# Kernel optimization log

Measured on AMD Instinct MI355X. Metric: run time of the kernel, lower is better.

Reference implementation:

```python
import jax, jax.numpy as jnp
import numpy as np

IMG_SIZE = 1024.0  # image width == height in pixels
N_PTS = 2_000_000


def setup_inputs() -> dict:
    key = jax.random.key(0)
    k1, k2, k3 = jax.random.split(key, 3)
    # 2D screen-space gaussian centers, pixel coords in [0, IMG_SIZE)
    pos2d = jax.random.uniform(k1, (N_PTS, 2), dtype=jnp.float32) * IMG_SIZE
    # PSD 2x2 covariances: A A^T + 0.5 I (screen-space extent of a few pixels)
    A = 0.8 * jax.random.normal(k2, (N_PTS, 2, 2), dtype=jnp.float32)
    cov2d = jnp.einsum('nij,nkj->nik', A, A) + 0.5 * jnp.eye(2, dtype=jnp.float32)
    opacity = jax.random.uniform(k3, (N_PTS,), dtype=jnp.float32)
    return {"pos2d": pos2d, "cov2d": cov2d, "opacity": opacity, "num_tile": 16}


def reference(pos2d, cov2d, opacity, num_tile):
    # --- per-gaussian rasterization setup (radius + conic) ---
    a = cov2d[:, 0, 0]; b = cov2d[:, 0, 1]
    c = cov2d[:, 1, 0]; d = cov2d[:, 1, 1]
    trace = a + d
    det = a * d - b * c
    term1 = 0.5 * trace
    term2 = 0.5 * jnp.sqrt(jnp.clip(trace * trace - 4.0 * det, 0.0))
    # max eigenvalue of the 2x2 covariance, as in GaussianRender.get_radius
    radius = jnp.maximum(term1 - term2, term1 + term2)
    inv_det = 1.0 / det
    conic = jnp.stack([d * inv_det, -b * inv_det, a * inv_det], axis=-1)  # [N,3]

    # --- tile binning (histogram) ---
    tile_size = IMG_SIZE / num_tile
    tile_xy = jnp.clip(jnp.floor(pos2d / tile_size).astype(jnp.int32), 0, num_tile - 1)
    tile_id = tile_xy[:, 1] * num_tile + tile_xy[:, 0]  # [N] in [0, num_tile^2)
    n_tiles = num_tile * num_tile
    tile_counts = jax.ops.segment_sum(
        jnp.ones_like(tile_id), tile_id, num_segments=n_tiles)  # [T^2]
    cum = jnp.cumsum(tile_counts)
    tile_offsets = jnp.concatenate([jnp.zeros((1,), cum.dtype), cum[:-1]])  # exclusive

    # --- counting sort: stable argsort by tile id reorders gaussians per tile ---
    order = jnp.argsort(tile_id)  # stable
    feat = jnp.concatenate(
        [pos2d, conic, opacity[:, None], radius[:, None]], axis=1)  # [N,7]
    sorted_feat = feat[order]
    return sorted_feat, tile_counts, tile_offsets, order.astype(jnp.int32)
```

## Files before the change

### kernel.cpp

```cpp
#include <hip/hip_runtime.h>

#define NT 16
#define NTILES 256
#define INV_TILE (1.0f/64.0f)
#define CHUNK 2048
#define THREADS 1024
#define NWAVES 16
#define FSTRIDE 2049

typedef float fv4 __attribute__((ext_vector_type(4)));

__device__ __forceinline__ int tile_of(float x, float y) {
    int tx = (int)floorf(x * INV_TILE);
    tx = tx < 0 ? 0 : (tx > NT - 1 ? NT - 1 : tx);
    int ty = (int)floorf(y * INV_TILE);
    ty = ty < 0 ? 0 : (ty > NT - 1 ? NT - 1 : ty);
    return ty * NT + tx;
}

__device__ __forceinline__ unsigned long long match_mask(int t, bool valid) {
    unsigned long long m = ~0ull;
#pragma unroll
    for (int b = 0; b < 8; ++b) {
        unsigned long long bal = __ballot((t >> b) & 1);
        m &= ((t >> b) & 1) ? bal : ~bal;
    }
    m &= __ballot(valid);
    return m;
}

__global__ __launch_bounds__(THREADS, 8) void k_hist(const float2* __restrict__ pos2d,
                                                     int* __restrict__ gTot,
                                                     int N) {
    __shared__ unsigned short cnt[NWAVES][NTILES];
    const int tid = threadIdx.x;
    const int wl = tid >> 6, lane = tid & 63;
    const int base_i = blockIdx.x * CHUNK;
    ((int*)cnt)[tid] = 0;
    ((int*)cnt)[tid + THREADS] = 0;
    __syncthreads();
#pragma unroll
    for (int r = 0; r < 2; ++r) {
        int o = wl * 128 + r * 64 + lane;
        int i = base_i + o;
        bool valid = i < N;
        int t = 0;
        if (valid) { float2 p = pos2d[i]; t = tile_of(p.x, p.y); }
        unsigned long long m = match_mask(t, valid);
        if (valid) {
            unsigned long long below = m & ((1ull << lane) - 1ull);
            if (below == 0ull)
                cnt[wl][t] = (unsigned short)(cnt[wl][t] + __popcll(m));
        }
    }
    __syncthreads();
    if (tid < NTILES) {
        int tot = 0;
#pragma unroll
        for (int w = 0; w < NWAVES; ++w) tot += cnt[w][tid];
        gTot[(size_t)blockIdx.x * NTILES + tid] = tot;
    }
}

__global__ __launch_bounds__(512) void k_scan(const int* __restrict__ gTot,
                                              int* __restrict__ gBaseT,
                                              int* __restrict__ gcnt,
                                              float* __restrict__ out_counts,
                                              int NWA) {
    const int t = blockIdx.x;
    const int tid = threadIdx.x;
    const int wl = tid >> 6, lane = tid & 63;
    __shared__ int wsum[8];

    int vals[4];
    const int base_row = tid * 4;
#pragma unroll
    for (int k = 0; k < 4; ++k) {
        int row = base_row + k;
        vals[k] = (row < NWA) ? gTot[(size_t)row * NTILES + t] : 0;
    }
    int tv = vals[0] + vals[1] + vals[2] + vals[3];
    int x = tv;
#pragma unroll
    for (int s = 1; s < 64; s <<= 1) {
        int y = __shfl_up(x, s);
        if (lane >= s) x += y;
    }
    if (lane == 63) wsum[wl] = x;
    __syncthreads();
    int wprefix = 0;
    for (int u = 0; u < wl; ++u) wprefix += wsum[u];
    int running = wprefix + (x - tv);
#pragma unroll
    for (int k = 0; k < 4; ++k) {
        int row = base_row + k;
        if (row < NWA) gBaseT[(size_t)t * NWA + row] = running;
        running += vals[k];
    }
    if (tid == 0) {
        int total = 0;
#pragma unroll
        for (int u = 0; u < 8; ++u) total += wsum[u];
        gcnt[t] = total;
        out_counts[t] = (float)total;
    }
}

__global__ __launch_bounds__(THREADS, 8) void k_scatter(const float2* __restrict__ pos2d,
                                                        const float4* __restrict__ cov2d,
                                                        const float*  __restrict__ opacity,
                                                        const int*    __restrict__ gBaseT,
                                                        const int*    __restrict__ gcnt,
                                                        float* __restrict__ out_feat,
                                                        float* __restrict__ out_offsets,
                                                        float* __restrict__ out_order,
                                                        int N, int NWA) {
    __shared__ float sFeat[7 * FSTRIDE];
    __shared__ unsigned int slotPk[CHUNK];
    __shared__ unsigned short cnt[NWAVES][NTILES];
    __shared__ int gbase[NTILES];
    __shared__ int base7[NTILES];
    __shared__ int obase[NTILES];
    __shared__ int wsum[NWAVES];

    const int tid = threadIdx.x;
    const int wl = tid >> 6, lane = tid & 63;
    const int b = blockIdx.x;

    const int nwg = gridDim.x;
    const int q = nwg >> 3, r = nwg & 7;
    const int xcd = b & 7, idx = b >> 3;
    const int chunk = (xcd < r ? xcd * (q + 1) : r * (q + 1) + (xcd - r) * q) + idx;
    const int base_i = chunk * CHUNK;

    ((int*)cnt)[tid] = 0;
    ((int*)cnt)[tid + THREADS] = 0;

    {
        int ct = 0, x = 0, gbt = 0;
        if (tid < NTILES) {
            gbt = gBaseT[(size_t)tid * NWA + chunk];
            ct = gcnt[tid];
            x = ct;
#pragma unroll
            for (int s = 1; s < 64; s <<= 1) {
                int y = __shfl_up(x, s);
                if (lane >= s) x += y;
            }
            if (lane == 63) wsum[wl] = x;
        }
        __syncthreads();
        if (tid < NTILES) {
            int wpre = 0;
            for (int u = 0; u < wl; ++u) wpre += wsum[u];
            int off = wpre + x - ct;
            gbase[tid] = off + gbt;
            if (b == 0) out_offsets[tid] = (float)off;
        }
    }
    __syncthreads();

    unsigned int meta[2];
#pragma unroll
    for (int r2 = 0; r2 < 2; ++r2) {
        int o = wl * 128 + r2 * 64 + lane;
        int i = base_i + o;
        bool valid = i < N;
        int t = 0;
        if (valid) {
            float2 p  = pos2d[i];
            fv4 cv = __builtin_nontemporal_load((const fv4*)cov2d + i);
            float op  = opacity[i];
            t = tile_of(p.x, p.y);
            float a = cv[0], bb = cv[1], d = cv[3];
            float trace = a + d;
            float det = a * d - bb * bb;
            float term1 = 0.5f * trace;
            float term2 = 0.5f * sqrtf(fmaxf(trace * trace - 4.0f * det, 0.0f));
            float rad = fmaxf(term1 - term2, term1 + term2);
            float inv = 1.0f / det;
            sFeat[0 * FSTRIDE + o] = p.x;
            sFeat[1 * FSTRIDE + o] = p.y;
            sFeat[2 * FSTRIDE + o] = d * inv;
            sFeat[3 * FSTRIDE + o] = -bb * inv;
            sFeat[4 * FSTRIDE + o] = a * inv;
            sFeat[5 * FSTRIDE + o] = op;
            sFeat[6 * FSTRIDE + o] = rad;
        }
        unsigned long long m = match_mask(t, valid);
        unsigned int pk = 0x80000000u;
        if (valid) {
            unsigned long long below = m & ((1ull << lane) - 1ull);
            int rank = __popcll(below);
            int b0 = cnt[wl][t];
            if (below == 0ull) cnt[wl][t] = (unsigned short)(b0 + __popcll(m));
            pk = ((unsigned)t << 16) | (unsigned)(b0 + rank);
        }
        meta[r2] = pk;
    }
    __syncthreads();

    int tot = 0, x = 0;
    if (tid < NTILES) {
#pragma unroll
        for (int w = 0; w < NWAVES; ++w) tot += cnt[w][tid];
        x = tot;
#pragma unroll
        for (int s = 1; s < 64; s <<= 1) {
            int y = __shfl_up(x, s);
            if (lane >= s) x += y;
        }
        if (lane == 63) wsum[wl] = x;
    }
    __syncthreads();
    if (tid < NTILES) {
        int wpre = 0;
        for (int u = 0; u < wl; ++u) wpre += wsum[u];
        int run = wpre + x - tot;
        int gb = gbase[tid];
        int ob = gb - run;
        obase[tid] = ob;
        base7[tid] = ob * 7;
#pragma unroll
        for (int w = 0; w < NWAVES; ++w) {
            int cw = cnt[w][tid];
            cnt[w][tid] = (unsigned short)run;
            run += cw;
        }
    }
    __syncthreads();

#pragma unroll
    for (int r2 = 0; r2 < 2; ++r2) {
        unsigned int pk = meta[r2];
        if (!(pk & 0x80000000u)) {
            int o = wl * 128 + r2 * 64 + lane;
            int t  = pk >> 16;
            int pw = pk & 0xFFFF;
            slotPk[cnt[wl][t] + pw] = ((unsigned)t << 16) | (unsigned)o;
        }
    }
    __syncthreads();

    int nvalid = N - base_i; if (nvalid > CHUNK) nvalid = CHUNK;
    int nv7 = nvalid * 7;
    {
        int j = (int)((unsigned)tid / 7u);
        int c = tid - 7 * j;
        for (int f = tid; f < nv7; f += THREADS) {
            unsigned int pk = slotPk[j];
            int t = pk >> 16;
            int o = pk & 0xFFFF;
            out_feat[(size_t)(base7[t] + f)] = sFeat[c * FSTRIDE + o];
            j += 146; c += 2;
            if (c >= 7) { c -= 7; j += 1; }
        }
    }
    for (int j2 = tid; j2 < nvalid; j2 += THREADS) {
        unsigned int pk = slotPk[j2];
        out_order[obase[pk >> 16] + j2] = (float)(base_i + (int)(pk & 0xFFFF));
    }
}

extern "C" void kernel_launch(void* const* d_in, const int* in_sizes, int n_in,
                              void* d_out, int out_size, void* d_ws, size_t ws_size,
                              hipStream_t stream) {
    const float2* pos2d   = (const float2*)d_in[0];
    const float4* cov2d   = (const float4*)d_in[1];
    const float*  opacity = (const float*)d_in[2];
    const int N = in_sizes[2];

    float* out         = (float*)d_out;
    float* out_feat    = out;
    float* out_counts  = out + (size_t)N * 7;
    float* out_offsets = out_counts + NTILES;
    float* out_order   = out_offsets + NTILES;

    int nchunks = (N + CHUNK - 1) / CHUNK;

    int* gTot   = (int*)d_ws;
    int* gBaseT = gTot + (size_t)nchunks * NTILES;
    int* gcnt   = gBaseT + (size_t)NTILES * nchunks;

    k_hist<<<nchunks, THREADS, 0, stream>>>(pos2d, gTot, N);
    k_scan<<<NTILES, 512, 0, stream>>>(gTot, gBaseT, gcnt, out_counts, nchunks);
    k_scatter<<<nchunks, THREADS, 0, stream>>>(pos2d, cov2d, opacity, gBaseT, gcnt,
                                               out_feat, out_offsets, out_order,
                                               N, nchunks);
}
```

Measured before the change: 131.9 us.

## Process two chunks per scatter block, prefetching the second chunk's inputs

```diff
diff --git a/kernel.cpp b/kernel.cpp
--- a/kernel.cpp
+++ b/kernel.cpp
@@ -105,6 +105,113 @@
         out_counts[t] = (float)total;
     }
 }
+
+#define PROCESS(PP, CC, OO, cc, PREFETCH)                                    \
+    {                                                                        \
+        const int base_i = (cc) * CHUNK;                                     \
+        ((int*)cnt)[tid] = 0;                                                \
+        ((int*)cnt)[tid + THREADS] = 0;                                      \
+        __syncthreads();   \
+        unsigned int meta[2];                                                \
+        _Pragma("unroll")                                                    \
+        for (int r2 = 0; r2 < 2; ++r2) {                                     \
+            int o = wl * 128 + r2 * 64 + lane;                               \
+            int i = base_i + o;                                              \
+            bool valid = ((cc) < NWA) && (i < N);                            \
+            int t = 0;                                                       \
+            if (valid) {                                                     \
+                float2 p = PP[r2]; fv4 cv = CC[r2]; float op = OO[r2];       \
+                t = tile_of(p.x, p.y);                                       \
+                float a = cv[0], bb2 = cv[1], d = cv[3];                     \
+                float trace = a + d;                                         \
+                float det = a * d - bb2 * bb2;       \
+                float term1 = 0.5f * trace;                                  \
+                float term2 = 0.5f * sqrtf(fmaxf(trace * trace - 4.0f * det, 0.0f)); \
+                float rad = fmaxf(term1 - term2, term1 + term2);             \
+                float inv = 1.0f / det;                                      \
+                sFeat[0 * FSTRIDE + o] = p.x;                                \
+                sFeat[1 * FSTRIDE + o] = p.y;                                \
+                sFeat[2 * FSTRIDE + o] = d * inv;                            \
+                sFeat[3 * FSTRIDE + o] = -bb2 * inv;                         \
+                sFeat[4 * FSTRIDE + o] = a * inv;                            \
+                sFeat[5 * FSTRIDE + o] = op;                                 \
+                sFeat[6 * FSTRIDE + o] = rad;                                \
+            }                                                                \
+            unsigned long long m = match_mask(t, valid);                     \
+            unsigned int pk = 0x80000000u;                                   \
+            if (valid) {                                                     \
+                unsigned long long below = m & ((1ull << lane) - 1ull);      \
+                int rank = __popcll(below);                                  \
+                int b0 = cnt[wl][t];         \
+                if (below == 0ull) cnt[wl][t] = (unsigned short)(b0 + __popcll(m)); \
+                pk = ((unsigned)t << 16) | (unsigned)(b0 + rank);            \
+            }                                                                \
+            meta[r2] = pk;                                                   \
+        }                                                                    \
+        __syncthreads();                                                     \
+        int tot = 0, x2 = 0;                                                 \
+        if (tid < NTILES) {                                                  \
+            _Pragma("unroll")                                                \
+            for (int w = 0; w < NWAVES; ++w) tot += cnt[w][tid];             \
+            x2 = tot;                                                        \
+            _Pragma("unroll")                                                \
+            for (int s = 1; s < 64; s <<= 1) {                               \
+                int y = __shfl_up(x2, s);                                    \
+                if (lane >= s) x2 += y;                                      \
+            }                                                                \
+            if (lane == 63) wsum[wl] = x2;                                   \
+        }                                                                    \
+        __syncthreads();                                                     \
+        if (tid < NTILES) {                                                  \
+            int wpre = 0;                                                    \
+            for (int u = 0; u < wl; ++u) wpre += wsum[u];                    \
+            int run = wpre + x2 - tot;                                       \
+            int gb = gbase[tid];                                             \
+            int ob = gb - run;                                               \
+            obase[tid] = ob;                                                 \
+            base7[tid] = ob * 7;                                             \
+            gbase[tid] = gb + tot;               \
+            _Pragma("unroll")                                                \
+            for (int w = 0; w < NWAVES; ++w) {                               \
+                int cw = cnt[w][tid];                                        \
+                cnt[w][tid] = (unsigned short)run;                           \
+                run += cw;                                                   \
+            }                                                                \
+        }                                                                    \
+        __syncthreads();                                                     \
+        _Pragma("unroll")                                                    \
+        for (int r2 = 0; r2 < 2; ++r2) {                                     \
+            unsigned int pk = meta[r2];                                      \
+            if (!(pk & 0x80000000u)) {                                       \
+                int o = wl * 128 + r2 * 64 + lane;                           \
+                int t = pk >> 16;                                            \
+                int pw = pk & 0xFFFF;                                        \
+                slotPk[cnt[wl][t] + pw] = ((unsigned)t << 16) | (unsigned)o; \
+            }                                                                \
+        }                                                                    \
+        __syncthreads();                                                     \
+        PREFETCH                                                             \
+        int nvalid = ((cc) < NWA) ? (N - base_i) : 0;                        \
+        if (nvalid > CHUNK) nvalid = CHUNK;                                  \
+        if (nvalid < 0) nvalid = 0;                                          \
+        int nv7 = nvalid * 7;                                                \
+        {                                                                    \
+            int j = (int)((unsigned)tid / 7u);   \
+            int c = tid - 7 * j;                                             \
+            for (int f = tid; f < nv7; f += THREADS) {                       \
+                unsigned int pk = slotPk[j];                                 \
+                int t = pk >> 16;                                            \
+                int o = pk & 0xFFFF;                                         \
+                out_feat[(size_t)(base7[t] + f)] = sFeat[c * FSTRIDE + o];   \
+                j += 146; c += 2;                                            \
+                if (c >= 7) { c -= 7; j += 1; }                              \
+            }                                                                \
+        }                                                                    \
+        for (int j2 = tid; j2 < nvalid; j2 += THREADS) {                     \
+            unsigned int pk = slotPk[j2];                                    \
+            out_order[obase[pk >> 16] + j2] = (float)(base_i + (int)(pk & 0xFFFF)); \
+        }                                                                    \
+    }
 
 __global__ __launch_bounds__(THREADS, 8) void k_scatter(const float2* __restrict__ pos2d,
                                                         const float4* __restrict__ cov2d,
@@ -130,16 +237,25 @@
     const int nwg = gridDim.x;
     const int q = nwg >> 3, r = nwg & 7;
     const int xcd = b & 7, idx = b >> 3;
-    const int chunk = (xcd < r ? xcd * (q + 1) : r * (q + 1) + (xcd - r) * q) + idx;
-    const int base_i = chunk * CHUNK;
-
-    ((int*)cnt)[tid] = 0;
-    ((int*)cnt)[tid + THREADS] = 0;
+    const int pair = (xcd < r ? xcd * (q + 1) : r * (q + 1) + (xcd - r) * q) + idx;
+    const int c0 = pair * 2;
+
+    float2 p0[2]; fv4 cv0[2]; float op0[2];
+    float2 p1[2]; fv4 cv1[2]; float op1[2];
+#pragma unroll
+    for (int r2 = 0; r2 < 2; ++r2) {
+        int i = c0 * CHUNK + wl * 128 + r2 * 64 + lane;
+        if (i < N) {
+            p0[r2]  = pos2d[i];
+            cv0[r2] = __builtin_nontemporal_load((const fv4*)cov2d + i);
+            op0[r2] = opacity[i];
+        }
+    }
 
     {
         int ct = 0, x = 0, gbt = 0;
         if (tid < NTILES) {
-            gbt = gBaseT[(size_t)tid * NWA + chunk];
+            gbt = gBaseT[(size_t)tid * NWA + c0];
             ct = gcnt[tid];
             x = ct;
 #pragma unroll
@@ -158,108 +274,20 @@
             if (b == 0) out_offsets[tid] = (float)off;
         }
     }
-    __syncthreads();
-
-    unsigned int meta[2];
-#pragma unroll
-    for (int r2 = 0; r2 < 2; ++r2) {
-        int o = wl * 128 + r2 * 64 + lane;
-        int i = base_i + o;
-        bool valid = i < N;
-        int t = 0;
-        if (valid) {
-            float2 p  = pos2d[i];
-            fv4 cv = __builtin_nontemporal_load((const fv4*)cov2d + i);
-            float op  = opacity[i];
-            t = tile_of(p.x, p.y);
-            float a = cv[0], bb = cv[1], d = cv[3];
-            float trace = a + d;
-            float det = a * d - bb * bb;
-            float term1 = 0.5f * trace;
-            float term2 = 0.5f * sqrtf(fmaxf(trace * trace - 4.0f * det, 0.0f));
-            float rad = fmaxf(term1 - term2, term1 + term2);
-            float inv = 1.0f / det;
-            sFeat[0 * FSTRIDE + o] = p.x;
-            sFeat[1 * FSTRIDE + o] = p.y;
-            sFeat[2 * FSTRIDE + o] = d * inv;
-            sFeat[3 * FSTRIDE + o] = -bb * inv;
-            sFeat[4 * FSTRIDE + o] = a * inv;
-            sFeat[5 * FSTRIDE + o] = op;
-            sFeat[6 * FSTRIDE + o] = rad;
-        }
-        unsigned long long m = match_mask(t, valid);
-        unsigned int pk = 0x80000000u;
-        if (valid) {
-            unsigned long long below = m & ((1ull << lane) - 1ull);
-            int rank = __popcll(below);
-            int b0 = cnt[wl][t];
-            if (below == 0ull) cnt[wl][t] = (unsigned short)(b0 + __popcll(m));
-            pk = ((unsigned)t << 16) | (unsigned)(b0 + rank);
-        }
-        meta[r2] = pk;
-    }
-    __syncthreads();
-
-    int tot = 0, x = 0;
-    if (tid < NTILES) {
-#pragma unroll
-        for (int w = 0; w < NWAVES; ++w) tot += cnt[w][tid];
-        x = tot;
-#pragma unroll
-        for (int s = 1; s < 64; s <<= 1) {
-            int y = __shfl_up(x, s);
-            if (lane >= s) x += y;
-        }
-        if (lane == 63) wsum[wl] = x;
-    }
-    __syncthreads();
-    if (tid < NTILES) {
-        int wpre = 0;
-        for (int u = 0; u < wl; ++u) wpre += wsum[u];
-        int run = wpre + x - tot;
-        int gb = gbase[tid];
-        int ob = gb - run;
-        obase[tid] = ob;
-        base7[tid] = ob * 7;
-#pragma unroll
-        for (int w = 0; w < NWAVES; ++w) {
-            int cw = cnt[w][tid];
-            cnt[w][tid] = (unsigned short)run;
-            run += cw;
-        }
-    }
-    __syncthreads();
-
-#pragma unroll
-    for (int r2 = 0; r2 < 2; ++r2) {
-        unsigned int pk = meta[r2];
-        if (!(pk & 0x80000000u)) {
-            int o = wl * 128 + r2 * 64 + lane;
-            int t  = pk >> 16;
-            int pw = pk & 0xFFFF;
-            slotPk[cnt[wl][t] + pw] = ((unsigned)t << 16) | (unsigned)o;
-        }
-    }
-    __syncthreads();
-
-    int nvalid = N - base_i; if (nvalid > CHUNK) nvalid = CHUNK;
-    int nv7 = nvalid * 7;
-    {
-        int j = (int)((unsigned)tid / 7u);
-        int c = tid - 7 * j;
-        for (int f = tid; f < nv7; f += THREADS) {
-            unsigned int pk = slotPk[j];
-            int t = pk >> 16;
-            int o = pk & 0xFFFF;
-            out_feat[(size_t)(base7[t] + f)] = sFeat[c * FSTRIDE + o];
-            j += 146; c += 2;
-            if (c >= 7) { c -= 7; j += 1; }
-        }
-    }
-    for (int j2 = tid; j2 < nvalid; j2 += THREADS) {
-        unsigned int pk = slotPk[j2];
-        out_order[obase[pk >> 16] + j2] = (float)(base_i + (int)(pk & 0xFFFF));
-    }
+
+    PROCESS(p0, cv0, op0, c0,
+        if (c0 + 1 < NWA) {
+            for (int r3 = 0; r3 < 2; ++r3) {
+                int i2 = (c0 + 1) * CHUNK + wl * 128 + r3 * 64 + lane;
+                if (i2 < N) {
+                    p1[r3]  = pos2d[i2];
+                    cv1[r3] = __builtin_nontemporal_load((const fv4*)cov2d + i2);
+                    op1[r3] = opacity[i2];
+                }
+            }
+        }
+    )
+    PROCESS(p1, cv1, op1, c0 + 1, )
 }
 
 extern "C" void kernel_launch(void* const* d_in, const int* in_sizes, int n_in,
@@ -277,6 +305,7 @@
     float* out_order   = out_offsets + NTILES;
 
     int nchunks = (N + CHUNK - 1) / CHUNK;
+    int npairs  = (nchunks + 1) / 2;
 
     int* gTot   = (int*)d_ws;
     int* gBaseT = gTot + (size_t)nchunks * NTILES;
@@ -284,7 +313,7 @@
 
     k_hist<<<nchunks, THREADS, 0, stream>>>(pos2d, gTot, N);
     k_scan<<<NTILES, 512, 0, stream>>>(gTot, gBaseT, gcnt, out_counts, nchunks);
-    k_scatter<<<nchunks, THREADS, 0, stream>>>(pos2d, cov2d, opacity, gBaseT, gcnt,
-                                               out_feat, out_offsets, out_order,
-                                               N, nchunks);
-}
+    k_scatter<<<npairs, THREADS, 0, stream>>>(pos2d, cov2d, opacity, gBaseT, gcnt,
+                                              out_feat, out_offsets, out_order,
+                                              N, nchunks);
+}
```

After: 135.5 us. 1.03x slower.
